# Kernel optimization log

Hardware: AMD Instinct MI355X
Metric: run time of the kernel (lower is better)

## Reference

```python
import jax, jax.numpy as jnp
import numpy as np

N = 100000      # nodes
E = 3200000     # edges
D_IN = 16
D_OUT = 32
DIM = 3         # pseudo-coordinate dimensionality
K = 2           # kernel_size per dim
NUM_K = K ** DIM  # 8 spline kernel weight matrices
BN_EPS = 1e-5


def _spline_basis(pseudo):
    """Degree-1 open B-spline basis, kernel_size=2 per dim.

    v = pseudo * (K - degree) = pseudo, so for pseudo in [0,1) floor(v)=0 and
    frac = pseudo; per-dim basis over the 2 knots is (1-frac, frac). The full
    basis over all 2^DIM kernel weights is the outer product across dims,
    flattened with flat index = i0 + 2*i1 + 4*i2.
    Returns [E, 2^DIM].
    """
    frac = pseudo  # [E, DIM]
    e = pseudo.shape[0]
    basis = jnp.ones((e, 1), pseudo.dtype)
    for d in range(DIM):
        b_d = jnp.stack([1.0 - frac[:, d], frac[:, d]], axis=1)  # [E, 2]
        # new flat index = i_d * prev_size + prev_index
        basis = (basis[:, None, :] * b_d[:, :, None]).reshape(e, -1)
    return basis  # [E, NUM_K]


def setup_inputs() -> dict:
    key = jax.random.key(0)
    ks = jax.random.split(key, 6)
    x = jax.random.normal(ks[0], (N, D_IN), dtype=jnp.float32)
    edge_index = jax.random.randint(ks[1], (2, E), 0, N, dtype=jnp.int32)
    edge_attr = jax.random.uniform(ks[2], (E, DIM), dtype=jnp.float32)
    # learned params
    W = jax.random.normal(ks[3], (NUM_K, D_IN, D_OUT), dtype=jnp.float32) * 0.1
    W_root = jax.random.normal(ks[4], (D_IN, D_OUT), dtype=jnp.float32) * 0.1
    bias = jnp.zeros((D_OUT,), jnp.float32)
    gamma = jnp.ones((D_OUT,), jnp.float32)
    beta = jnp.zeros((D_OUT,), jnp.float32)
    return dict(x=x, edge_index=edge_index, edge_attr=edge_attr,
                W=W, W_root=W_root, bias=bias, gamma=gamma, beta=beta)


def reference(x, edge_index, edge_attr, W, W_root, bias, gamma, beta):
    src, dst = edge_index[0], edge_index[1]
    basis = _spline_basis(edge_attr)          # [E, 8]
    x_j = x[src]                              # [E, d_in] per-edge gather
    # basis-weighted linear combination over the 8 kernel weights
    msg = jnp.zeros((x_j.shape[0], D_OUT), x.dtype)
    for k in range(NUM_K):                    # fixed small loop over kernels
        msg = msg + basis[:, k:k + 1] * (x_j @ W[k])
    # scatter-mean to target nodes (SplineConv default aggr='mean')
    agg = jax.ops.segment_sum(msg, dst, num_segments=N)
    cnt = jax.ops.segment_sum(jnp.ones((msg.shape[0],), x.dtype), dst, num_segments=N)
    agg = agg / jnp.maximum(cnt, 1.0)[:, None]
    out = agg + x @ W_root + bias             # root weight + bias
    out = jax.nn.elu(out)                     # activation
    # BatchNorm over the node dimension (training mode: batch statistics)
    mean = out.mean(axis=0)
    var = out.var(axis=0)
    out = (out - mean) * jax.lax.rsqrt(var + BN_EPS) * gamma + beta
    return out
```

## Files before the change

kernel.cpp:

```cpp
#include <hip/hip_runtime.h>
#include <math.h>

#define TPB 256
#define FTPB 512
#define D_IN 16
#define D_OUT 32
#define NUM_K 8
#define WPAD 516
#define SBN_LOG 9
#define SBN 512
#define CT 4096
#define EPT 16


__global__ void k_zero256(int* __restrict__ sbcnt) {
    sbcnt[threadIdx.x] = 0;
}

__global__ void k_sbhist(const int* __restrict__ dst, int* __restrict__ sbcnt, int E) {
    __shared__ int h[256];
    for (int i = threadIdx.x; i < 256; i += TPB) h[i] = 0;
    __syncthreads();
    int stride = gridDim.x * TPB;
    for (int e = blockIdx.x * TPB + threadIdx.x; e < E; e += stride)
        atomicAdd(&h[dst[e] >> SBN_LOG], 1);
    __syncthreads();
    for (int i = threadIdx.x; i < 256; i += TPB)
        if (h[i]) atomicAdd(&sbcnt[i], h[i]);
}

__global__ void k_sbscan(const int* __restrict__ sbcnt, int* __restrict__ sbo,
                         int* __restrict__ scursor, int nsb, int E) {
    __shared__ int sd[256];
    int t = threadIdx.x;
    int own = (t < nsb) ? sbcnt[t] : 0;
    sd[t] = own;
    __syncthreads();
    for (int s = 1; s < 256; s <<= 1) {
        int add = (t >= s) ? sd[t - s] : 0;
        __syncthreads();
        sd[t] += add;
        __syncthreads();
    }
    if (t < nsb) { sbo[t] = sd[t] - own; scursor[t] = sd[t] - own; }
    if (t == 0) sbo[nsb] = E;
}

__global__ __launch_bounds__(TPB) void k_coarse(
        const int* __restrict__ src, const int* __restrict__ dst,
        const float* __restrict__ attr, int* __restrict__ scursor,
        uint2* __restrict__ tmp, int E, int nsb) {
    __shared__ int hist[256];
    __shared__ int base[256];
    __shared__ int goff[256];
    __shared__ __align__(16) uint2 stage[CT];
    __shared__ unsigned char ssb[CT];

    int tile0 = blockIdx.x * CT;
    for (int i = threadIdx.x; i < 256; i += TPB) hist[i] = 0;
    __syncthreads();

    unsigned rx[EPT], ry[EPT];
    int rk[EPT], sbv[EPT];
#pragma unroll
    for (int i = 0; i < EPT; i++) {
        int e = tile0 + i * TPB + threadIdx.x;
        sbv[i] = -1;
        if (e < E) {
            int s = src[e], d = dst[e];
            float f0 = attr[3 * e + 0], f1 = attr[3 * e + 1], f2 = attr[3 * e + 2];
            int q0 = min((int)(f0 * 1024.f), 1023);
            int q1 = min((int)(f1 * 1024.f), 1023);
            int q2 = min((int)(f2 * 1024.f), 1023);
            int sb = d >> SBN_LOG;
            rx[i] = (unsigned)s | ((unsigned)(d & (SBN - 1)) << 17);
            ry[i] = (unsigned)q0 | ((unsigned)q1 << 10) | ((unsigned)q2 << 20);
            rk[i] = atomicAdd(&hist[sb], 1);
            sbv[i] = sb;
        }
    }
    __syncthreads();

    int t = threadIdx.x;
    int cntv = hist[t];
    base[t] = cntv;
    __syncthreads();
    for (int s = 1; s < 256; s <<= 1) {
        int add = (t >= s) ? base[t - s] : 0;
        __syncthreads();
        base[t] += add;
        __syncthreads();
    }
    int excl = base[t] - cntv;
    if (t < nsb && cntv > 0) goff[t] = atomicAdd(&scursor[t], cntv);
    __syncthreads();
    base[t] = excl;
    __syncthreads();

#pragma unroll
    for (int i = 0; i < EPT; i++) {
        if (sbv[i] >= 0) {
            int slot = base[sbv[i]] + rk[i];
            stage[slot] = make_uint2(rx[i], ry[i]);
            ssb[slot] = (unsigned char)sbv[i];
        }
    }
    __syncthreads();

    int tileCount = min(E - tile0, CT);
    for (int j = threadIdx.x; j < tileCount; j += TPB) {
        int sb = ssb[j];
        tmp[goff[sb] + (j - base[sb])] = stage[j];
    }
}

__global__ __launch_bounds__(FTPB) void k_fine2(
        const uint2* __restrict__ tmp, const int* __restrict__ sbo,
        int* __restrict__ cursor, uint2* __restrict__ rec, int N) {
    __shared__ int hist[SBN];
    __shared__ int scan[SBN];
    int b = blockIdx.x;
    int lo = sbo[b], hi = sbo[b + 1];
    int t = threadIdx.x;
    hist[t] = 0;
    __syncthreads();
    for (int p = lo + t; p < hi; p += FTPB)
        atomicAdd(&hist[(tmp[p].x >> 17) & (SBN - 1)], 1);
    __syncthreads();
    int own = hist[t];
    scan[t] = own;
    __syncthreads();
    for (int s = 1; s < SBN; s <<= 1) {
        int add = (t >= s) ? scan[t - s] : 0;
        __syncthreads();
        scan[t] += add;
        __syncthreads();
    }
    int incl = scan[t];
    int n = (b << SBN_LOG) + t;
    if (n < N) cursor[n] = lo + incl;
    __syncthreads();
    hist[t] = lo + incl - own;
    __syncthreads();
    for (int p = lo + t; p < hi; p += FTPB) {
        uint2 r = tmp[p];
        int dl = (int)((r.x >> 17) & (SBN - 1));
        int slot = atomicAdd(&hist[dl], 1);
        rec[slot] = make_uint2(r.x & 0x1FFFFu, r.y);
    }
}


__global__ void k_zero(int* __restrict__ cnt, int N) {
    int i = blockIdx.x * TPB + threadIdx.x;
    if (i < N) cnt[i] = 0;
}

__global__ void k_hist(const int* __restrict__ dst, int* __restrict__ cnt, int E) {
    int e = blockIdx.x * TPB + threadIdx.x;
    if (e < E) atomicAdd(&cnt[dst[e]], 1);
}

__global__ void k_scan_a(const int* __restrict__ cnt, int* __restrict__ bsum, int N) {
    __shared__ int sd[TPB];
    int i = blockIdx.x * TPB + threadIdx.x;
    sd[threadIdx.x] = (i < N) ? cnt[i] : 0;
    __syncthreads();
    for (int s = TPB / 2; s > 0; s >>= 1) {
        if (threadIdx.x < s) sd[threadIdx.x] += sd[threadIdx.x + s];
        __syncthreads();
    }
    if (threadIdx.x == 0) bsum[blockIdx.x] = sd[0];
}

__global__ void k_scan_b(const int* __restrict__ bsum, int* __restrict__ boff, int nb) {
    __shared__ int sd[512];
    int t = threadIdx.x;
    int own = (t < nb) ? bsum[t] : 0;
    sd[t] = own;
    __syncthreads();
    for (int s = 1; s < 512; s <<= 1) {
        int a = sd[t];
        int b = (t >= s) ? sd[t - s] : 0;
        __syncthreads();
        sd[t] = a + b;
        __syncthreads();
    }
    if (t < nb) boff[t] = sd[t] - own;
}

__global__ void k_scan_c(const int* __restrict__ cnt, const int* __restrict__ boff,
                         int* __restrict__ cursor, int N) {
    __shared__ int sd[TPB];
    int t = threadIdx.x;
    int i = blockIdx.x * TPB + t;
    int v = (i < N) ? cnt[i] : 0;
    sd[t] = v;
    __syncthreads();
    for (int s = 1; s < TPB; s <<= 1) {
        int a = sd[t];
        int b = (t >= s) ? sd[t - s] : 0;
        __syncthreads();
        sd[t] = a + b;
        __syncthreads();
    }
    if (i < N) cursor[i] = sd[t] - v + boff[blockIdx.x];
}

__global__ void k_scatter(const int* __restrict__ src, const int* __restrict__ dst,
                          const float* __restrict__ attr, int* __restrict__ cursor,
                          uint2* __restrict__ rec, int E) {
    int e = blockIdx.x * TPB + threadIdx.x;
    if (e < E) {
        float f0 = attr[3 * e + 0], f1 = attr[3 * e + 1], f2 = attr[3 * e + 2];
        int q0 = min((int)(f0 * 1024.f), 1023);
        int q1 = min((int)(f1 * 1024.f), 1023);
        int q2 = min((int)(f2 * 1024.f), 1023);
        unsigned pk = (unsigned)q0 | ((unsigned)q1 << 10) | ((unsigned)q2 << 20);
        int pos = atomicAdd(&cursor[dst[e]], 1);
        rec[pos] = make_uint2((unsigned)src[e], pk);
    }
}


__global__ __launch_bounds__(TPB, 4) void k_agg(
    const float* __restrict__ x, const float* __restrict__ W,
    const float* __restrict__ Wr, const float* __restrict__ bias,
    const int* __restrict__ cursor, const uint2* __restrict__ rec,
    float* __restrict__ out, float* __restrict__ partials, int N) {

    __shared__ __align__(16) float sW[NUM_K * WPAD];
    __shared__ __align__(16) float sWr[D_IN * D_OUT];
    __shared__ float sB[D_OUT];
    __shared__ float4 sStats[4][16];

    for (int idx = threadIdx.x; idx < NUM_K * D_IN * D_OUT; idx += TPB) {
        int k = idx >> 9, rem = idx & 511, i = rem >> 5, c = rem & 31;
        sW[k * WPAD + i * 32 + c] = W[idx];
    }
    for (int idx = threadIdx.x; idx < D_IN * D_OUT; idx += TPB) sWr[idx] = Wr[idx];
    if (threadIdx.x < D_OUT) sB[threadIdx.x] = bias[threadIdx.x];
    __syncthreads();

    int t   = blockIdx.x * TPB + threadIdx.x;
    int n   = t >> 4;
    int sub = t & 15;
    int grp = sub >> 3;
    int h   = sub & 7;
    bool valid = n < N;

    float4 g0 = {0,0,0,0}, g1 = {0,0,0,0}, g2 = {0,0,0,0}, g3 = {0,0,0,0};
    int deg = 0;
    if (valid) {
        int p0 = (n == 0) ? 0 : cursor[n - 1];
        int p1 = cursor[n];
        deg = p1 - p0;
        int p = p0 + grp;
        if (p < p1) {
            int last = p1 - 1;
            uint2 r  = rec[p];
            uint2 rn = rec[min(p + 2, last)];
            const float4* xr = (const float4*)x + (size_t)r.x * 4;
            float4 xq0 = xr[0], xq1 = xr[1], xq2 = xr[2], xq3 = xr[3];
            for (; p < p1; p += 2) {
                uint2 rnn = rec[min(p + 4, last)];
                const float4* xnr = (const float4*)x + (size_t)rn.x * 4;
                float4 xn0 = xnr[0], xn1 = xnr[1], xn2 = xnr[2], xn3 = xnr[3];
                float f0 = ((float)(r.y & 1023u) + 0.5f) * (1.f / 1024.f);
                float f1 = ((float)((r.y >> 10) & 1023u) + 0.5f) * (1.f / 1024.f);
                float f2 = ((float)((r.y >> 20) & 1023u) + 0.5f) * (1.f / 1024.f);
                float b0 = (h & 1) ? f0 : 1.f - f0;
                float b1 = (h & 2) ? f1 : 1.f - f1;
                float b2 = (h & 4) ? f2 : 1.f - f2;
                float bs = b0 * b1 * b2;
                g0.x = fmaf(bs, xq0.x, g0.x); g0.y = fmaf(bs, xq0.y, g0.y);
                g0.z = fmaf(bs, xq0.z, g0.z); g0.w = fmaf(bs, xq0.w, g0.w);
                g1.x = fmaf(bs, xq1.x, g1.x); g1.y = fmaf(bs, xq1.y, g1.y);
                g1.z = fmaf(bs, xq1.z, g1.z); g1.w = fmaf(bs, xq1.w, g1.w);
                g2.x = fmaf(bs, xq2.x, g2.x); g2.y = fmaf(bs, xq2.y, g2.y);
                g2.z = fmaf(bs, xq2.z, g2.z); g2.w = fmaf(bs, xq2.w, g2.w);
                g3.x = fmaf(bs, xq3.x, g3.x); g3.y = fmaf(bs, xq3.y, g3.y);
                g3.z = fmaf(bs, xq3.z, g3.z); g3.w = fmaf(bs, xq3.w, g3.w);
                r = rn; rn = rnn;
                xq0 = xn0; xq1 = xn1; xq2 = xn2; xq3 = xn3;
            }
        }
    }

    g0.x += __shfl_xor(g0.x, 8); g0.y += __shfl_xor(g0.y, 8);
    g0.z += __shfl_xor(g0.z, 8); g0.w += __shfl_xor(g0.w, 8);
    g1.x += __shfl_xor(g1.x, 8); g1.y += __shfl_xor(g1.y, 8);
    g1.z += __shfl_xor(g1.z, 8); g1.w += __shfl_xor(g1.w, 8);
    g2.x += __shfl_xor(g2.x, 8); g2.y += __shfl_xor(g2.y, 8);
    g2.z += __shfl_xor(g2.z, 8); g2.w += __shfl_xor(g2.w, 8);
    g3.x += __shfl_xor(g3.x, 8); g3.y += __shfl_xor(g3.y, 8);
    g3.z += __shfl_xor(g3.z, 8); g3.w += __shfl_xor(g3.w, 8);

    float4 o0 = {0,0,0,0}, o1 = {0,0,0,0}, o2 = {0,0,0,0}, o3 = {0,0,0,0};
    const float* wbase = sW + h * WPAD + grp * 16;
#define CONTRACT1(gv, i) { \
        const float4* wr_ = (const float4*)(wbase + (i) * 32); \
        float4 w0 = wr_[0], w1 = wr_[1], w2 = wr_[2], w3 = wr_[3]; \
        o0.x = fmaf(gv, w0.x, o0.x); o0.y = fmaf(gv, w0.y, o0.y); \
        o0.z = fmaf(gv, w0.z, o0.z); o0.w = fmaf(gv, w0.w, o0.w); \
        o1.x = fmaf(gv, w1.x, o1.x); o1.y = fmaf(gv, w1.y, o1.y); \
        o1.z = fmaf(gv, w1.z, o1.z); o1.w = fmaf(gv, w1.w, o1.w); \
        o2.x = fmaf(gv, w2.x, o2.x); o2.y = fmaf(gv, w2.y, o2.y); \
        o2.z = fmaf(gv, w2.z, o2.z); o2.w = fmaf(gv, w2.w, o2.w); \
        o3.x = fmaf(gv, w3.x, o3.x); o3.y = fmaf(gv, w3.y, o3.y); \
        o3.z = fmaf(gv, w3.z, o3.z); o3.w = fmaf(gv, w3.w, o3.w); }
    CONTRACT1(g0.x,  0) CONTRACT1(g0.y,  1) CONTRACT1(g0.z,  2) CONTRACT1(g0.w,  3)
    CONTRACT1(g1.x,  4) CONTRACT1(g1.y,  5) CONTRACT1(g1.z,  6) CONTRACT1(g1.w,  7)
    CONTRACT1(g2.x,  8) CONTRACT1(g2.y,  9) CONTRACT1(g2.z, 10) CONTRACT1(g2.w, 11)
    CONTRACT1(g3.x, 12) CONTRACT1(g3.y, 13) CONTRACT1(g3.z, 14) CONTRACT1(g3.w, 15)
#undef CONTRACT1

    float inv = 1.f / (float)(deg > 0 ? deg : 1);
    o0.x *= inv; o0.y *= inv; o0.z *= inv; o0.w *= inv;
    o1.x *= inv; o1.y *= inv; o1.z *= inv; o1.w *= inv;
    o2.x *= inv; o2.y *= inv; o2.z *= inv; o2.w *= inv;
    o3.x *= inv; o3.y *= inv; o3.z *= inv; o3.w *= inv;

    bool hi4 = (h & 4) != 0;
    float4 k0, k1, s0, s1;
    k0 = hi4 ? o2 : o0; k1 = hi4 ? o3 : o1;
    s0 = hi4 ? o0 : o2; s1 = hi4 ? o1 : o3;
    k0.x += __shfl_xor(s0.x, 4); k0.y += __shfl_xor(s0.y, 4);
    k0.z += __shfl_xor(s0.z, 4); k0.w += __shfl_xor(s0.w, 4);
    k1.x += __shfl_xor(s1.x, 4); k1.y += __shfl_xor(s1.y, 4);
    k1.z += __shfl_xor(s1.z, 4); k1.w += __shfl_xor(s1.w, 4);

    bool hi2 = (h & 2) != 0;
    float4 m0 = hi2 ? k1 : k0;
    float4 sm = hi2 ? k0 : k1;
    m0.x += __shfl_xor(sm.x, 2); m0.y += __shfl_xor(sm.y, 2);
    m0.z += __shfl_xor(sm.z, 2); m0.w += __shfl_xor(sm.w, 2);

    bool hi1 = (h & 1) != 0;
    float e0 = hi1 ? m0.z : m0.x;
    float e1 = hi1 ? m0.w : m0.y;
    float sa = hi1 ? m0.x : m0.z;
    float sb_ = hi1 ? m0.y : m0.w;
    e0 += __shfl_xor(sa, 1);
    e1 += __shfl_xor(sb_, 1);

    int c0 = 2 * sub;
    if (valid) {
        const float4* xr = (const float4*)x + (size_t)n * 4;
        float4 r0 = xr[0], r1 = xr[1], r2 = xr[2], r3 = xr[3];
#define ROOT1(xv, i) { \
            float2 w = *(const float2*)(sWr + (i) * 32 + c0); \
            e0 = fmaf(xv, w.x, e0); e1 = fmaf(xv, w.y, e1); }
        ROOT1(r0.x,  0) ROOT1(r0.y,  1) ROOT1(r0.z,  2) ROOT1(r0.w,  3)
        ROOT1(r1.x,  4) ROOT1(r1.y,  5) ROOT1(r1.z,  6) ROOT1(r1.w,  7)
        ROOT1(r2.x,  8) ROOT1(r2.y,  9) ROOT1(r2.z, 10) ROOT1(r2.w, 11)
        ROOT1(r3.x, 12) ROOT1(r3.y, 13) ROOT1(r3.z, 14) ROOT1(r3.w, 15)
#undef ROOT1
    }

    float2 bb = *(const float2*)(sB + c0);
    e0 += bb.x; e1 += bb.y;
    e0 = e0 > 0.f ? e0 : (expf(e0) - 1.f);
    e1 = e1 > 0.f ? e1 : (expf(e1) - 1.f);

    if (valid) *(float2*)(out + (size_t)n * D_OUT + c0) = make_float2(e0, e1);

    float ss0 = valid ? e0 : 0.f, ss1 = valid ? e1 : 0.f;
    float q0 = ss0 * ss0, q1 = ss1 * ss1;
    ss0 += __shfl_xor(ss0, 16); ss1 += __shfl_xor(ss1, 16);
    q0  += __shfl_xor(q0, 16);  q1  += __shfl_xor(q1, 16);
    ss0 += __shfl_xor(ss0, 32); ss1 += __shfl_xor(ss1, 32);
    q0  += __shfl_xor(q0, 32);  q1  += __shfl_xor(q1, 32);
    if ((threadIdx.x & 63) < 16)
        sStats[threadIdx.x >> 6][sub] = make_float4(ss0, ss1, q0, q1);
    __syncthreads();
    if (threadIdx.x < 64) {
        const float* sf = (const float*)sStats;
        float v = sf[threadIdx.x] + sf[64 + threadIdx.x] +
                  sf[128 + threadIdx.x] + sf[192 + threadIdx.x];
        int ssub = threadIdx.x >> 2, comp = threadIdx.x & 3;
        int col = 2 * ssub + (comp & 1) + 32 * (comp >> 1);
        partials[(size_t)blockIdx.x * 64 + col] = v;
    }
}


__global__ void k_red1(const float* __restrict__ partials, float* __restrict__ partials2,
                       int nrows) {
    __shared__ float sd[4][64];
    int col = threadIdx.x & 63, j = threadIdx.x >> 6;
    float v = 0.f;
    for (int k = 0; k < 16; k++) {
        int r = blockIdx.x * 64 + j * 16 + k;
        if (r < nrows) v += partials[(size_t)r * 64 + col];
    }
    sd[j][col] = v;
    __syncthreads();
    if (threadIdx.x < 64)
        partials2[(size_t)blockIdx.x * 64 + threadIdx.x] =
            sd[0][threadIdx.x] + sd[1][threadIdx.x] + sd[2][threadIdx.x] + sd[3][threadIdx.x];
}

__global__ void k_bnfin(const float* __restrict__ partials2, const float* __restrict__ gamma,
                        const float* __restrict__ beta, float* __restrict__ stats,
                        int nrows2, int N) {
    __shared__ float sd[2][64];
    int col = threadIdx.x & 63, j = threadIdx.x >> 6;
    float v = 0.f;
    for (int r = j; r < nrows2; r += 2) v += partials2[(size_t)r * 64 + col];
    sd[j][col] = v;
    __syncthreads();
    if (threadIdx.x < 32) {
        int c = threadIdx.x;
        float S = sd[0][c] + sd[1][c];
        float Q = sd[0][32 + c] + sd[1][32 + c];
        float mean = S / (float)N;
        float var  = Q / (float)N - mean * mean;
        float sc   = gamma[c] * rsqrtf(var + 1e-5f);
        stats[c]      = sc;
        stats[32 + c] = beta[c] - mean * sc;
    }
}

__global__ void k_bnapply(float* __restrict__ out, const float* __restrict__ stats, int total4) {
    int i = blockIdx.x * TPB + threadIdx.x;
    if (i < total4) {
        float4 v = ((float4*)out)[i];
        int c0 = (i * 4) & (D_OUT - 1);
        v.x = v.x * stats[c0 + 0] + stats[32 + c0 + 0];
        v.y = v.y * stats[c0 + 1] + stats[32 + c0 + 1];
        v.z = v.z * stats[c0 + 2] + stats[32 + c0 + 2];
        v.w = v.w * stats[c0 + 3] + stats[32 + c0 + 3];
        ((float4*)out)[i] = v;
    }
}


extern "C" void kernel_launch(void* const* d_in, const int* in_sizes, int n_in,
                              void* d_out, int out_size, void* d_ws, size_t ws_size,
                              hipStream_t stream) {
    const float* x     = (const float*)d_in[0];
    const int* eidx    = (const int*)d_in[1];
    const float* attr  = (const float*)d_in[2];
    const float* W     = (const float*)d_in[3];
    const float* Wr    = (const float*)d_in[4];
    const float* bias  = (const float*)d_in[5];
    const float* gamma = (const float*)d_in[6];
    const float* beta  = (const float*)d_in[7];
    float* out = (float*)d_out;

    const int N = in_sizes[0] / D_IN;
    const int E = in_sizes[1] / 2;
    const int* src = eidx;
    const int* dst = eidx + E;

    const int nb  = (N + TPB - 1) / TPB;
    const int gE  = (E + TPB - 1) / TPB;
    const int nsb = (N + SBN - 1) / SBN;
    const int nbAgg = (16 * N + TPB - 1) / TPB;
    const int nbRed = (nbAgg + 63) / 64;
    const int gC  = (E + CT - 1) / CT;

    uint2* rec       = (uint2*)d_ws;
    int* cursor      = (int*)(rec + E);
    float* partials  = (float*)(cursor + N);
    float* partials2 = partials + (size_t)nbAgg * 64;
    float* stats     = partials2 + (size_t)nbRed * 64;
    int* sbcnt       = (int*)(stats + 64);
    int* sbo         = sbcnt + 256;
    int* scursor     = sbo + 257;
    uintptr_t tail   = ((uintptr_t)(scursor + 256) + 15) & ~(uintptr_t)15;
    uint2* tmp       = (uint2*)tail;
    size_t need_primary  = (tail + (size_t)E * 8) - (uintptr_t)d_ws;
    size_t need_fallback = (tail + ((size_t)N + 2 * nb) * 4) - (uintptr_t)d_ws;
    bool primary = (ws_size >= need_primary) && (nsb <= 256) && (nb <= 512);

    if (primary) {
        k_zero256<<<1, 256, 0, stream>>>(sbcnt);
        int gH = min(1024, gE);
        k_sbhist<<<gH, TPB, 0, stream>>>(dst, sbcnt, E);
        k_sbscan<<<1, 256, 0, stream>>>(sbcnt, sbo, scursor, nsb, E);
        k_coarse<<<gC, TPB, 0, stream>>>(src, dst, attr, scursor, tmp, E, nsb);
        k_fine2<<<nsb, FTPB, 0, stream>>>(tmp, sbo, cursor, rec, N);
    } else if (ws_size >= need_fallback && nb <= 512) {
        int* cnt  = (int*)tail;
        int* bsum = cnt + N;
        int* boff = bsum + nb;
        k_zero<<<nb, TPB, 0, stream>>>(cnt, N);
        k_hist<<<gE, TPB, 0, stream>>>(dst, cnt, E);
        k_scan_a<<<nb, TPB, 0, stream>>>(cnt, bsum, N);
        k_scan_b<<<1, 512, 0, stream>>>(bsum, boff, nb);
        k_scan_c<<<nb, TPB, 0, stream>>>(cnt, boff, cursor, N);
        k_scatter<<<gE, TPB, 0, stream>>>(src, dst, attr, cursor, rec, E);
    }

    k_agg<<<nbAgg, TPB, 0, stream>>>(x, W, Wr, bias, cursor, rec, out, partials, N);
    k_red1<<<nbRed, TPB, 0, stream>>>(partials, partials2, nbAgg);
    k_bnfin<<<1, 128, 0, stream>>>(partials2, gamma, beta, stats, nbRed, N);
    int total4 = N * D_OUT / 4;
    k_bnapply<<<(total4 + TPB - 1) / TPB, TPB, 0, stream>>>(out, stats, total4);
}
```

Measured before the change: 212.0 us.

## Sort nodes by degree before aggregation and restructure edge loop into paired loads

```diff
diff --git a/kernel.cpp b/kernel.cpp
--- a/kernel.cpp
+++ b/kernel.cpp
@@ -13,8 +13,8 @@
 #define EPT 16
 
 
-__global__ void k_zero256(int* __restrict__ sbcnt) {
-    sbcnt[threadIdx.x] = 0;
+__global__ void k_zero256(int* __restrict__ p) {
+    p[threadIdx.x] = 0;
 }
 
 __global__ void k_sbhist(const int* __restrict__ dst, int* __restrict__ sbcnt, int E) {
@@ -151,6 +151,58 @@
 }
 
 
+__global__ void k_deghist(const int* __restrict__ cursor, int* __restrict__ dcnt, int N) {
+    __shared__ int h[256];
+    h[threadIdx.x] = 0;
+    __syncthreads();
+    int stride = gridDim.x * TPB;
+    for (int n = blockIdx.x * TPB + threadIdx.x; n < N; n += stride) {
+        int p1 = cursor[n];
+        int p0 = (n == 0) ? 0 : cursor[n - 1];
+        atomicAdd(&h[min(p1 - p0, 255)], 1);
+    }
+    __syncthreads();
+    if (h[threadIdx.x]) atomicAdd(&dcnt[threadIdx.x], h[threadIdx.x]);
+}
+
+__global__ void k_degscan(const int* __restrict__ dcnt, int* __restrict__ dcur) {
+    __shared__ int sd[256];
+    int t = threadIdx.x;
+    int own = dcnt[t];
+    sd[t] = own;
+    __syncthreads();
+    for (int s = 1; s < 256; s <<= 1) {
+        int add = (t >= s) ? sd[t - s] : 0;
+        __syncthreads();
+        sd[t] += add;
+        __syncthreads();
+    }
+    dcur[t] = sd[t] - own;
+}
+
+__global__ void k_degscatter(const int* __restrict__ cursor, int* __restrict__ dcur,
+                             int* __restrict__ perm, int N) {
+    __shared__ int h[256];
+    __shared__ int base[256];
+    int t = threadIdx.x;
+    h[t] = 0;
+    __syncthreads();
+    int n = blockIdx.x * TPB + t;
+    int bin = -1, rank = 0;
+    if (n < N) {
+        int p1 = cursor[n];
+        int p0 = (n == 0) ? 0 : cursor[n - 1];
+        bin = min(p1 - p0, 255);
+        rank = atomicAdd(&h[bin], 1);
+    }
+    __syncthreads();
+    int c = h[t];
+    if (c) base[t] = atomicAdd(&dcur[t], c);
+    __syncthreads();
+    if (n < N) perm[base[bin] + rank] = n;
+}
+
+
 __global__ void k_zero(int* __restrict__ cnt, int N) {
     int i = blockIdx.x * TPB + threadIdx.x;
     if (i < N) cnt[i] = 0;
@@ -227,6 +279,7 @@
     const float* __restrict__ x, const float* __restrict__ W,
     const float* __restrict__ Wr, const float* __restrict__ bias,
     const int* __restrict__ cursor, const uint2* __restrict__ rec,
+    const int* __restrict__ perm,
     float* __restrict__ out, float* __restrict__ partials, int N) {
 
     __shared__ __align__(16) float sW[NUM_K * WPAD];
@@ -242,12 +295,13 @@
     if (threadIdx.x < D_OUT) sB[threadIdx.x] = bias[threadIdx.x];
     __syncthreads();
 
-    int t   = blockIdx.x * TPB + threadIdx.x;
-    int n   = t >> 4;
-    int sub = t & 15;
-    int grp = sub >> 3;
-    int h   = sub & 7;
-    bool valid = n < N;
+    int t    = blockIdx.x * TPB + threadIdx.x;
+    int slot = t >> 4;
+    int sub  = t & 15;
+    int grp  = sub >> 3;
+    int h    = sub & 7;
+    bool valid = slot < N;
+    int n = valid ? perm[slot] : 0;
 
     float4 g0 = {0,0,0,0}, g1 = {0,0,0,0}, g2 = {0,0,0,0}, g3 = {0,0,0,0};
     int deg = 0;
@@ -256,34 +310,47 @@
         int p1 = cursor[n];
         deg = p1 - p0;
         int p = p0 + grp;
-        if (p < p1) {
-            int last = p1 - 1;
-            uint2 r  = rec[p];
-            uint2 rn = rec[min(p + 2, last)];
-            const float4* xr = (const float4*)x + (size_t)r.x * 4;
-            float4 xq0 = xr[0], xq1 = xr[1], xq2 = xr[2], xq3 = xr[3];
-            for (; p < p1; p += 2) {
-                uint2 rnn = rec[min(p + 4, last)];
-                const float4* xnr = (const float4*)x + (size_t)rn.x * 4;
-                float4 xn0 = xnr[0], xn1 = xnr[1], xn2 = xnr[2], xn3 = xnr[3];
-                float f0 = ((float)(r.y & 1023u) + 0.5f) * (1.f / 1024.f);
-                float f1 = ((float)((r.y >> 10) & 1023u) + 0.5f) * (1.f / 1024.f);
-                float f2 = ((float)((r.y >> 20) & 1023u) + 0.5f) * (1.f / 1024.f);
-                float b0 = (h & 1) ? f0 : 1.f - f0;
-                float b1 = (h & 2) ? f1 : 1.f - f1;
-                float b2 = (h & 4) ? f2 : 1.f - f2;
-                float bs = b0 * b1 * b2;
-                g0.x = fmaf(bs, xq0.x, g0.x); g0.y = fmaf(bs, xq0.y, g0.y);
-                g0.z = fmaf(bs, xq0.z, g0.z); g0.w = fmaf(bs, xq0.w, g0.w);
-                g1.x = fmaf(bs, xq1.x, g1.x); g1.y = fmaf(bs, xq1.y, g1.y);
-                g1.z = fmaf(bs, xq1.z, g1.z); g1.w = fmaf(bs, xq1.w, g1.w);
-                g2.x = fmaf(bs, xq2.x, g2.x); g2.y = fmaf(bs, xq2.y, g2.y);
-                g2.z = fmaf(bs, xq2.z, g2.z); g2.w = fmaf(bs, xq2.w, g2.w);
-                g3.x = fmaf(bs, xq3.x, g3.x); g3.y = fmaf(bs, xq3.y, g3.y);
-                g3.z = fmaf(bs, xq3.z, g3.z); g3.w = fmaf(bs, xq3.w, g3.w);
-                r = rn; rn = rnn;
-                xq0 = xn0; xq1 = xn1; xq2 = xn2; xq3 = xn3;
-            }
+        while (p < p1) {
+            uint2 rA = rec[p];
+            bool hasB = (p + 2) < p1;
+            uint2 rB = hasB ? rec[p + 2] : rA;
+            const float4* xa = (const float4*)x + (size_t)rA.x * 4;
+            const float4* xb = (const float4*)x + (size_t)rB.x * 4;
+            float4 a0 = xa[0], a1 = xa[1], a2 = xa[2], a3 = xa[3];
+            float4 c0v = xb[0], c1v = xb[1], c2v = xb[2], c3v = xb[3];
+
+            float fA0 = ((float)(rA.y & 1023u) + 0.5f) * (1.f / 1024.f);
+            float fA1 = ((float)((rA.y >> 10) & 1023u) + 0.5f) * (1.f / 1024.f);
+            float fA2 = ((float)((rA.y >> 20) & 1023u) + 0.5f) * (1.f / 1024.f);
+            float bsA = ((h & 1) ? fA0 : 1.f - fA0) *
+                        ((h & 2) ? fA1 : 1.f - fA1) *
+                        ((h & 4) ? fA2 : 1.f - fA2);
+            g0.x = fmaf(bsA, a0.x, g0.x); g0.y = fmaf(bsA, a0.y, g0.y);
+            g0.z = fmaf(bsA, a0.z, g0.z); g0.w = fmaf(bsA, a0.w, g0.w);
+            g1.x = fmaf(bsA, a1.x, g1.x); g1.y = fmaf(bsA, a1.y, g1.y);
+            g1.z = fmaf(bsA, a1.z, g1.z); g1.w = fmaf(bsA, a1.w, g1.w);
+            g2.x = fmaf(bsA, a2.x, g2.x); g2.y = fmaf(bsA, a2.y, g2.y);
+            g2.z = fmaf(bsA, a2.z, g2.z); g2.w = fmaf(bsA, a2.w, g2.w);
+            g3.x = fmaf(bsA, a3.x, g3.x); g3.y = fmaf(bsA, a3.y, g3.y);
+            g3.z = fmaf(bsA, a3.z, g3.z); g3.w = fmaf(bsA, a3.w, g3.w);
+
+            float fB0 = ((float)(rB.y & 1023u) + 0.5f) * (1.f / 1024.f);
+            float fB1 = ((float)((rB.y >> 10) & 1023u) + 0.5f) * (1.f / 1024.f);
+            float fB2 = ((float)((rB.y >> 20) & 1023u) + 0.5f) * (1.f / 1024.f);
+            float bsB = ((h & 1) ? fB0 : 1.f - fB0) *
+                        ((h & 2) ? fB1 : 1.f - fB1) *
+                        ((h & 4) ? fB2 : 1.f - fB2);
+            bsB = hasB ? bsB : 0.f;
+            g0.x = fmaf(bsB, c0v.x, g0.x); g0.y = fmaf(bsB, c0v.y, g0.y);
+            g0.z = fmaf(bsB, c0v.z, g0.z); g0.w = fmaf(bsB, c0v.w, g0.w);
+            g1.x = fmaf(bsB, c1v.x, g1.x); g1.y = fmaf(bsB, c1v.y, g1.y);
+            g1.z = fmaf(bsB, c1v.z, g1.z); g1.w = fmaf(bsB, c1v.w, g1.w);
+            g2.x = fmaf(bsB, c2v.x, g2.x); g2.y = fmaf(bsB, c2v.y, g2.y);
+            g2.z = fmaf(bsB, c2v.z, g2.z); g2.w = fmaf(bsB, c2v.w, g2.w);
+            g3.x = fmaf(bsB, c3v.x, g3.x); g3.y = fmaf(bsB, c3v.y, g3.y);
+            g3.z = fmaf(bsB, c3v.z, g3.z); g3.w = fmaf(bsB, c3v.w, g3.w);
+
+            p += 4;
         }
     }
 
@@ -463,13 +530,16 @@
 
     uint2* rec       = (uint2*)d_ws;
     int* cursor      = (int*)(rec + E);
-    float* partials  = (float*)(cursor + N);
+    int* perm        = cursor + N;
+    float* partials  = (float*)(perm + N);
     float* partials2 = partials + (size_t)nbAgg * 64;
     float* stats     = partials2 + (size_t)nbRed * 64;
     int* sbcnt       = (int*)(stats + 64);
     int* sbo         = sbcnt + 256;
     int* scursor     = sbo + 257;
-    uintptr_t tail   = ((uintptr_t)(scursor + 256) + 15) & ~(uintptr_t)15;
+    int* dcnt        = scursor + 256;
+    int* dcur        = dcnt + 256;
+    uintptr_t tail   = ((uintptr_t)(dcur + 256) + 15) & ~(uintptr_t)15;
     uint2* tmp       = (uint2*)tail;
     size_t need_primary  = (tail + (size_t)E * 8) - (uintptr_t)d_ws;
     size_t need_fallback = (tail + ((size_t)N + 2 * nb) * 4) - (uintptr_t)d_ws;
@@ -494,7 +564,12 @@
         k_scatter<<<gE, TPB, 0, stream>>>(src, dst, attr, cursor, rec, E);
     }
 
-    k_agg<<<nbAgg, TPB, 0, stream>>>(x, W, Wr, bias, cursor, rec, out, partials, N);
+    k_zero256<<<1, 256, 0, stream>>>(dcnt);
+    k_deghist<<<min(nb, 512), TPB, 0, stream>>>(cursor, dcnt, N);
+    k_degscan<<<1, 256, 0, stream>>>(dcnt, dcur);
+    k_degscatter<<<nb, TPB, 0, stream>>>(cursor, dcur, perm, N);
+
+    k_agg<<<nbAgg, TPB, 0, stream>>>(x, W, Wr, bias, cursor, rec, perm, out, partials, N);
     k_red1<<<nbRed, TPB, 0, stream>>>(partials, partials2, nbAgg);
     k_bnfin<<<1, 128, 0, stream>>>(partials2, gamma, beta, stats, nbRed, N);
     int total4 = N * D_OUT / 4;
```

New measurement: 239.0 us. 1.13x slower.

## Use fixed-capacity strided bucket layout to drop histogram and scan passes

Applied to the files above, without the earlier changes.

```diff
diff --git a/kernel.cpp b/kernel.cpp
--- a/kernel.cpp
+++ b/kernel.cpp
@@ -12,10 +12,13 @@
 #define CT 4096
 #define EPT 16
 
-
-__global__ void k_zero256(int* __restrict__ sbcnt) {
-    sbcnt[threadIdx.x] = 0;
-}
+__global__ void k_init(int* __restrict__ sbase, int* __restrict__ scursor,
+                       int* __restrict__ sbcnt, int cap, int strided) {
+    int t = threadIdx.x;
+    if (t < 257) sbase[t] = strided ? t * cap : 0;
+    if (t < 256) { scursor[t] = 0; sbcnt[t] = 0; }
+}
+
 
 __global__ void k_sbhist(const int* __restrict__ dst, int* __restrict__ sbcnt, int E) {
     __shared__ int h[256];
@@ -29,8 +32,7 @@
         if (h[i]) atomicAdd(&sbcnt[i], h[i]);
 }
 
-__global__ void k_sbscan(const int* __restrict__ sbcnt, int* __restrict__ sbo,
-                         int* __restrict__ scursor, int nsb, int E) {
+__global__ void k_sbscan(const int* __restrict__ sbcnt, int* __restrict__ sbase, int nsb) {
     __shared__ int sd[256];
     int t = threadIdx.x;
     int own = (t < nsb) ? sbcnt[t] : 0;
@@ -42,14 +44,13 @@
         sd[t] += add;
         __syncthreads();
     }
-    if (t < nsb) { sbo[t] = sd[t] - own; scursor[t] = sd[t] - own; }
-    if (t == 0) sbo[nsb] = E;
+    sbase[t] = sd[t] - own;
 }
 
 __global__ __launch_bounds__(TPB) void k_coarse(
         const int* __restrict__ src, const int* __restrict__ dst,
-        const float* __restrict__ attr, int* __restrict__ scursor,
-        uint2* __restrict__ tmp, int E, int nsb) {
+        const float* __restrict__ attr, const int* __restrict__ sbase,
+        int* __restrict__ scursor, uint2* __restrict__ tmp, int E, int nsb) {
     __shared__ int hist[256];
     __shared__ int base[256];
     __shared__ int goff[256];
@@ -92,7 +93,7 @@
         __syncthreads();
     }
     int excl = base[t] - cntv;
-    if (t < nsb && cntv > 0) goff[t] = atomicAdd(&scursor[t], cntv);
+    if (t < nsb && cntv > 0) goff[t] = sbase[t] + atomicAdd(&scursor[t], cntv);
     __syncthreads();
     base[t] = excl;
     __syncthreads();
@@ -115,12 +116,14 @@
 }
 
 __global__ __launch_bounds__(FTPB) void k_fine2(
-        const uint2* __restrict__ tmp, const int* __restrict__ sbo,
-        int* __restrict__ cursor, uint2* __restrict__ rec, int N) {
+        const uint2* __restrict__ tmp, const int* __restrict__ sbase,
+        const int* __restrict__ scursor, int* __restrict__ rs, int* __restrict__ re,
+        uint2* __restrict__ rec, int N) {
     __shared__ int hist[SBN];
-    __shared__ int scan[SBN];
+    __shared__ int wsum[8], woff[8];
     int b = blockIdx.x;
-    int lo = sbo[b], hi = sbo[b + 1];
+    int lo = sbase[b];
+    int hi = lo + scursor[b];
     int t = threadIdx.x;
     hist[t] = 0;
     __syncthreads();
@@ -128,19 +131,32 @@
         atomicAdd(&hist[(tmp[p].x >> 17) & (SBN - 1)], 1);
     __syncthreads();
     int own = hist[t];
-    scan[t] = own;
-    __syncthreads();
-    for (int s = 1; s < SBN; s <<= 1) {
-        int add = (t >= s) ? scan[t - s] : 0;
-        __syncthreads();
-        scan[t] += add;
-        __syncthreads();
-    }
-    int incl = scan[t];
+
+    int lane = t & 63, w = t >> 6;
+    int inc = own;
+#pragma unroll
+    for (int s = 1; s < 64; s <<= 1) {
+        int u = __shfl_up(inc, s);
+        if (lane >= s) inc += u;
+    }
+    if (lane == 63) wsum[w] = inc;
+    __syncthreads();
+    if (t < 8) {
+        int x = wsum[t], ex = x;
+#pragma unroll
+        for (int s = 1; s < 8; s <<= 1) {
+            int u = __shfl_up(ex, s);
+            if (t >= s) ex += u;
+        }
+        woff[t] = ex - x;
+    }
+    __syncthreads();
+    int incl = inc + woff[w];
+    int excl = incl - own;
+
     int n = (b << SBN_LOG) + t;
-    if (n < N) cursor[n] = lo + incl;
-    __syncthreads();
-    hist[t] = lo + incl - own;
+    if (n < N) { rs[n] = lo + excl; re[n] = lo + incl; }
+    hist[t] = lo + excl;
     __syncthreads();
     for (int p = lo + t; p < hi; p += FTPB) {
         uint2 r = tmp[p];
@@ -190,7 +206,7 @@
 }
 
 __global__ void k_scan_c(const int* __restrict__ cnt, const int* __restrict__ boff,
-                         int* __restrict__ cursor, int N) {
+                         int* __restrict__ rs, int* __restrict__ re, int N) {
     __shared__ int sd[TPB];
     int t = threadIdx.x;
     int i = blockIdx.x * TPB + t;
@@ -204,11 +220,12 @@
         sd[t] = a + b;
         __syncthreads();
     }
-    if (i < N) cursor[i] = sd[t] - v + boff[blockIdx.x];
+    int excl = sd[t] - v + boff[blockIdx.x];
+    if (i < N) { rs[i] = excl; re[i] = excl; }
 }
 
 __global__ void k_scatter(const int* __restrict__ src, const int* __restrict__ dst,
-                          const float* __restrict__ attr, int* __restrict__ cursor,
+                          const float* __restrict__ attr, int* __restrict__ re,
                           uint2* __restrict__ rec, int E) {
     int e = blockIdx.x * TPB + threadIdx.x;
     if (e < E) {
@@ -217,7 +234,7 @@
         int q1 = min((int)(f1 * 1024.f), 1023);
         int q2 = min((int)(f2 * 1024.f), 1023);
         unsigned pk = (unsigned)q0 | ((unsigned)q1 << 10) | ((unsigned)q2 << 20);
-        int pos = atomicAdd(&cursor[dst[e]], 1);
+        int pos = atomicAdd(&re[dst[e]], 1);
         rec[pos] = make_uint2((unsigned)src[e], pk);
     }
 }
@@ -226,7 +243,8 @@
 __global__ __launch_bounds__(TPB, 4) void k_agg(
     const float* __restrict__ x, const float* __restrict__ W,
     const float* __restrict__ Wr, const float* __restrict__ bias,
-    const int* __restrict__ cursor, const uint2* __restrict__ rec,
+    const int* __restrict__ rs, const int* __restrict__ re,
+    const uint2* __restrict__ rec,
     float* __restrict__ out, float* __restrict__ partials, int N) {
 
     __shared__ __align__(16) float sW[NUM_K * WPAD];
@@ -249,41 +267,54 @@
     int h   = sub & 7;
     bool valid = n < N;
 
+    const float INV = 1.0f / 1024.0f, HLF = 1.0f / 2048.0f;
+    float sc0 = (h & 1) ? INV : -INV, cc0 = (h & 1) ? HLF : 1.f - HLF;
+    float sc1 = (h & 2) ? INV : -INV, cc1 = (h & 2) ? HLF : 1.f - HLF;
+    float sc2 = (h & 4) ? INV : -INV, cc2 = (h & 4) ? HLF : 1.f - HLF;
+
     float4 g0 = {0,0,0,0}, g1 = {0,0,0,0}, g2 = {0,0,0,0}, g3 = {0,0,0,0};
     int deg = 0;
     if (valid) {
-        int p0 = (n == 0) ? 0 : cursor[n - 1];
-        int p1 = cursor[n];
+        int p0 = rs[n], p1 = re[n];
         deg = p1 - p0;
         int p = p0 + grp;
-        if (p < p1) {
-            int last = p1 - 1;
-            uint2 r  = rec[p];
-            uint2 rn = rec[min(p + 2, last)];
-            const float4* xr = (const float4*)x + (size_t)r.x * 4;
-            float4 xq0 = xr[0], xq1 = xr[1], xq2 = xr[2], xq3 = xr[3];
-            for (; p < p1; p += 2) {
-                uint2 rnn = rec[min(p + 4, last)];
-                const float4* xnr = (const float4*)x + (size_t)rn.x * 4;
-                float4 xn0 = xnr[0], xn1 = xnr[1], xn2 = xnr[2], xn3 = xnr[3];
-                float f0 = ((float)(r.y & 1023u) + 0.5f) * (1.f / 1024.f);
-                float f1 = ((float)((r.y >> 10) & 1023u) + 0.5f) * (1.f / 1024.f);
-                float f2 = ((float)((r.y >> 20) & 1023u) + 0.5f) * (1.f / 1024.f);
-                float b0 = (h & 1) ? f0 : 1.f - f0;
-                float b1 = (h & 2) ? f1 : 1.f - f1;
-                float b2 = (h & 4) ? f2 : 1.f - f2;
-                float bs = b0 * b1 * b2;
-                g0.x = fmaf(bs, xq0.x, g0.x); g0.y = fmaf(bs, xq0.y, g0.y);
-                g0.z = fmaf(bs, xq0.z, g0.z); g0.w = fmaf(bs, xq0.w, g0.w);
-                g1.x = fmaf(bs, xq1.x, g1.x); g1.y = fmaf(bs, xq1.y, g1.y);
-                g1.z = fmaf(bs, xq1.z, g1.z); g1.w = fmaf(bs, xq1.w, g1.w);
-                g2.x = fmaf(bs, xq2.x, g2.x); g2.y = fmaf(bs, xq2.y, g2.y);
-                g2.z = fmaf(bs, xq2.z, g2.z); g2.w = fmaf(bs, xq2.w, g2.w);
-                g3.x = fmaf(bs, xq3.x, g3.x); g3.y = fmaf(bs, xq3.y, g3.y);
-                g3.z = fmaf(bs, xq3.z, g3.z); g3.w = fmaf(bs, xq3.w, g3.w);
-                r = rn; rn = rnn;
-                xq0 = xn0; xq1 = xn1; xq2 = xn2; xq3 = xn3;
-            }
+        while (p < p1) {
+            uint2 rA = rec[p];
+            bool hasB = (p + 2) < p1;
+            uint2 rB = hasB ? rec[p + 2] : rA;
+            const float4* xa = (const float4*)x + (size_t)rA.x * 4;
+            const float4* xb = (const float4*)x + (size_t)rB.x * 4;
+            float4 a0 = xa[0], a1 = xa[1], a2 = xa[2], a3 = xa[3];
+            float4 c0v = xb[0], c1v = xb[1], c2v = xb[2], c3v = xb[3];
+
+            float qA0 = (float)(rA.y & 1023u);
+            float qA1 = (float)((rA.y >> 10) & 1023u);
+            float qA2 = (float)((rA.y >> 20) & 1023u);
+            float bsA = fmaf(qA0, sc0, cc0) * fmaf(qA1, sc1, cc1) * fmaf(qA2, sc2, cc2);
+            g0.x = fmaf(bsA, a0.x, g0.x); g0.y = fmaf(bsA, a0.y, g0.y);
+            g0.z = fmaf(bsA, a0.z, g0.z); g0.w = fmaf(bsA, a0.w, g0.w);
+            g1.x = fmaf(bsA, a1.x, g1.x); g1.y = fmaf(bsA, a1.y, g1.y);
+            g1.z = fmaf(bsA, a1.z, g1.z); g1.w = fmaf(bsA, a1.w, g1.w);
+            g2.x = fmaf(bsA, a2.x, g2.x); g2.y = fmaf(bsA, a2.y, g2.y);
+            g2.z = fmaf(bsA, a2.z, g2.z); g2.w = fmaf(bsA, a2.w, g2.w);
+            g3.x = fmaf(bsA, a3.x, g3.x); g3.y = fmaf(bsA, a3.y, g3.y);
+            g3.z = fmaf(bsA, a3.z, g3.z); g3.w = fmaf(bsA, a3.w, g3.w);
+
+            float qB0 = (float)(rB.y & 1023u);
+            float qB1 = (float)((rB.y >> 10) & 1023u);
+            float qB2 = (float)((rB.y >> 20) & 1023u);
+            float bsB = fmaf(qB0, sc0, cc0) * fmaf(qB1, sc1, cc1) * fmaf(qB2, sc2, cc2);
+            bsB = hasB ? bsB : 0.f;
+            g0.x = fmaf(bsB, c0v.x, g0.x); g0.y = fmaf(bsB, c0v.y, g0.y);
+            g0.z = fmaf(bsB, c0v.z, g0.z); g0.w = fmaf(bsB, c0v.w, g0.w);
+            g1.x = fmaf(bsB, c1v.x, g1.x); g1.y = fmaf(bsB, c1v.y, g1.y);
+            g1.z = fmaf(bsB, c1v.z, g1.z); g1.w = fmaf(bsB, c1v.w, g1.w);
+            g2.x = fmaf(bsB, c2v.x, g2.x); g2.y = fmaf(bsB, c2v.y, g2.y);
+            g2.z = fmaf(bsB, c2v.z, g2.z); g2.w = fmaf(bsB, c2v.w, g2.w);
+            g3.x = fmaf(bsB, c3v.x, g3.x); g3.y = fmaf(bsB, c3v.y, g3.y);
+            g3.z = fmaf(bsB, c3v.z, g3.z); g3.w = fmaf(bsB, c3v.w, g3.w);
+
+            p += 4;
         }
     }
 
@@ -360,8 +391,8 @@
 
     float2 bb = *(const float2*)(sB + c0);
     e0 += bb.x; e1 += bb.y;
-    e0 = e0 > 0.f ? e0 : (expf(e0) - 1.f);
-    e1 = e1 > 0.f ? e1 : (expf(e1) - 1.f);
+    e0 = e0 > 0.f ? e0 : (__expf(e0) - 1.f);
+    e1 = e1 > 0.f ? e1 : (__expf(e1) - 1.f);
 
     if (valid) *(float2*)(out + (size_t)n * D_OUT + c0) = make_float2(e0, e1);
 
@@ -461,40 +492,57 @@
     const int nbRed = (nbAgg + 63) / 64;
     const int gC  = (E + CT - 1) / CT;
 
-    uint2* rec       = (uint2*)d_ws;
-    int* cursor      = (int*)(rec + E);
-    float* partials  = (float*)(cursor + N);
+    int capBase = (E + nsb - 1) / nsb;
+    int slack = capBase / 16 > 1024 ? capBase / 16 : 1024;
+    int cap = capBase + slack;
+
+    int* rs          = (int*)d_ws;
+    int* re          = rs + N;
+    float* partials  = (float*)(re + N);
     float* partials2 = partials + (size_t)nbAgg * 64;
     float* stats     = partials2 + (size_t)nbRed * 64;
-    int* sbcnt       = (int*)(stats + 64);
-    int* sbo         = sbcnt + 256;
-    int* scursor     = sbo + 257;
-    uintptr_t tail   = ((uintptr_t)(scursor + 256) + 15) & ~(uintptr_t)15;
-    uint2* tmp       = (uint2*)tail;
-    size_t need_primary  = (tail + (size_t)E * 8) - (uintptr_t)d_ws;
-    size_t need_fallback = (tail + ((size_t)N + 2 * nb) * 4) - (uintptr_t)d_ws;
-    bool primary = (ws_size >= need_primary) && (nsb <= 256) && (nb <= 512);
-
-    if (primary) {
-        k_zero256<<<1, 256, 0, stream>>>(sbcnt);
+    int* sbase       = (int*)(stats + 64);
+    int* scursor     = sbase + 257;
+    int* sbcnt       = scursor + 256;
+    uintptr_t tail   = ((uintptr_t)(sbcnt + 256) + 15) & ~(uintptr_t)15;
+    size_t headBytes = tail - (uintptr_t)d_ws;
+
+    size_t recStr      = (size_t)nsb * cap;
+    size_t needStrided = headBytes + 2 * recStr * 8;
+    size_t needDense   = headBytes + 2 * (size_t)E * 8;
+    size_t needSingle  = headBytes + (size_t)E * 8 + ((size_t)N + 2 * (size_t)nb) * 4;
+
+    if (ws_size >= needStrided && nsb <= 256) {
+        uint2* rec = (uint2*)tail;
+        uint2* tmp = rec + recStr;
+        k_init<<<1, 512, 0, stream>>>(sbase, scursor, sbcnt, cap, 1);
+        k_coarse<<<gC, TPB, 0, stream>>>(src, dst, attr, sbase, scursor, tmp, E, nsb);
+        k_fine2<<<nsb, FTPB, 0, stream>>>(tmp, sbase, scursor, rs, re, rec, N);
+        k_agg<<<nbAgg, TPB, 0, stream>>>(x, W, Wr, bias, rs, re, rec, out, partials, N);
+    } else if (ws_size >= needDense && nsb <= 256) {
+        uint2* rec = (uint2*)tail;
+        uint2* tmp = rec + E;
+        k_init<<<1, 512, 0, stream>>>(sbase, scursor, sbcnt, cap, 0);
         int gH = min(1024, gE);
         k_sbhist<<<gH, TPB, 0, stream>>>(dst, sbcnt, E);
-        k_sbscan<<<1, 256, 0, stream>>>(sbcnt, sbo, scursor, nsb, E);
-        k_coarse<<<gC, TPB, 0, stream>>>(src, dst, attr, scursor, tmp, E, nsb);
-        k_fine2<<<nsb, FTPB, 0, stream>>>(tmp, sbo, cursor, rec, N);
-    } else if (ws_size >= need_fallback && nb <= 512) {
-        int* cnt  = (int*)tail;
-        int* bsum = cnt + N;
-        int* boff = bsum + nb;
+        k_sbscan<<<1, 256, 0, stream>>>(sbcnt, sbase, nsb);
+        k_coarse<<<gC, TPB, 0, stream>>>(src, dst, attr, sbase, scursor, tmp, E, nsb);
+        k_fine2<<<nsb, FTPB, 0, stream>>>(tmp, sbase, scursor, rs, re, rec, N);
+        k_agg<<<nbAgg, TPB, 0, stream>>>(x, W, Wr, bias, rs, re, rec, out, partials, N);
+    } else if (ws_size >= needSingle && nb <= 512) {
+        uint2* rec = (uint2*)tail;
+        int* cnt   = (int*)(rec + E);
+        int* bsum  = cnt + N;
+        int* boff  = bsum + nb;
         k_zero<<<nb, TPB, 0, stream>>>(cnt, N);
         k_hist<<<gE, TPB, 0, stream>>>(dst, cnt, E);
         k_scan_a<<<nb, TPB, 0, stream>>>(cnt, bsum, N);
         k_scan_b<<<1, 512, 0, stream>>>(bsum, boff, nb);
-        k_scan_c<<<nb, TPB, 0, stream>>>(cnt, boff, cursor, N);
-        k_scatter<<<gE, TPB, 0, stream>>>(src, dst, attr, cursor, rec, E);
-    }
-
-    k_agg<<<nbAgg, TPB, 0, stream>>>(x, W, Wr, bias, cursor, rec, out, partials, N);
+        k_scan_c<<<nb, TPB, 0, stream>>>(cnt, boff, rs, re, N);
+        k_scatter<<<gE, TPB, 0, stream>>>(src, dst, attr, re, rec, E);
+        k_agg<<<nbAgg, TPB, 0, stream>>>(x, W, Wr, bias, rs, re, rec, out, partials, N);
+    }
+
     k_red1<<<nbRed, TPB, 0, stream>>>(partials, partials2, nbAgg);
     k_bnfin<<<1, 128, 0, stream>>>(partials2, gamma, beta, stats, nbRed, N);
     int total4 = N * D_OUT / 4;
```

Result: slower. 217.2 us (+2.5%).
